# Kernel tuning notes

Measured on AMD Instinct MI355X. Metric: run time of the kernel, lower is better.

## Reference

```python
import jax, jax.numpy as jnp
import numpy as np

VOCAB = 1024   # must equal HID (embedding Linear consumes vocab-sized x)
HID = 1024
EMB = 256
NOS = 12
B, M = 512, 8
TEMP = 1.0


def setup_inputs() -> dict:
    key = jax.random.key(0)
    ks = jax.random.split(key, 12)
    N = B * M
    target = jax.random.normal(ks[0], (B, M, HID), jnp.float32)
    # precomputed standard Gumbel noise per step (training=True path)
    u = jax.random.uniform(ks[1], (NOS, N, VOCAB), jnp.float32, 1e-6, 1.0 - 1e-6)
    gumbels = -jnp.log(-jnp.log(u))
    sh = 1.0 / np.sqrt(HID)
    sv = 1.0 / np.sqrt(VOCAB)
    sos = 0.01 * jax.random.normal(ks[2], (EMB,), jnp.float32)
    W_ih = jax.random.uniform(ks[3], (HID, EMB), jnp.float32, -sh, sh)
    b_ih = jax.random.uniform(ks[4], (HID,), jnp.float32, -sh, sh)
    W_hh = jax.random.uniform(ks[5], (HID, HID), jnp.float32, -sh, sh)
    b_hh = jax.random.uniform(ks[6], (HID,), jnp.float32, -sh, sh)
    W_out = jax.random.uniform(ks[7], (VOCAB, HID), jnp.float32, -sh, sh)
    b_out = jax.random.uniform(ks[8], (VOCAB,), jnp.float32, -sh, sh)
    W_emb = jax.random.uniform(ks[9], (EMB, VOCAB), jnp.float32, -sv, sv)
    b_emb = jax.random.uniform(ks[10], (EMB,), jnp.float32, -sv, sv)
    return dict(target=target, gumbels=gumbels, sos=sos,
                W_ih=W_ih, b_ih=b_ih, W_hh=W_hh, b_hh=b_hh,
                W_out=W_out, b_out=b_out, W_emb=W_emb, b_emb=b_emb)


def reference(target, gumbels, sos, W_ih, b_ih, W_hh, b_hh, W_out, b_out, W_emb, b_emb):
    b_, m_, h_ = target.shape
    prev = target.reshape(b_ * m_, h_)            # [N, HID]
    e0 = jnp.broadcast_to(sos, (prev.shape[0], sos.shape[0]))  # [N, EMB]

    def step(carry, g):
        prev_h, e = carry
        h = jnp.tanh(e @ W_ih.T + b_ih + prev_h @ W_hh.T + b_hh)   # RNNCell
        logits = h @ W_out.T + b_out                               # [N, VOCAB]
        x = jax.nn.softmax((logits + g) / TEMP, axis=-1)           # gumbel-softmax
        e_next = x @ W_emb.T + b_emb                               # [N, EMB]
        return (h, e_next), x

    _, xs = jax.lax.scan(step, (prev, e0), gumbels)  # xs: [NOS, N, VOCAB]
    return jnp.transpose(xs, (1, 0, 2))              # [N, NOS, VOCAB]
```

## Files before the change

kernel.cpp:

```cpp
#include <hip/hip_runtime.h>

#define N_TOT 4096
#define HIDN  1024
#define EMBD  256
#define VOC   1024
#define NSTEP 12

typedef __bf16 bf16;
typedef _Float16 h16;
typedef __bf16 bf16x8 __attribute__((ext_vector_type(8)));
typedef __bf16 bf16x4 __attribute__((ext_vector_type(4)));
typedef _Float16 h16x8 __attribute__((ext_vector_type(8)));
typedef float  f32x4  __attribute__((ext_vector_type(4)));

static __device__ __forceinline__ f32x4 mfma16(bf16x8 a, bf16x8 b, f32x4 c) {
  return __builtin_amdgcn_mfma_f32_16x16x32_bf16(a, b, c, 0, 0, 0);
}

static __device__ __forceinline__ void gload16(const bf16* g, bf16* l) {
  __builtin_amdgcn_global_load_lds(
      (const __attribute__((address_space(1))) void*)g,
      (__attribute__((address_space(3))) void*)l, 16, 0, 0);
}


__global__ void cvt_kernel(const float* __restrict__ s, bf16* __restrict__ d, int n) {
  for (int i = blockIdx.x * blockDim.x + threadIdx.x; i < n; i += blockDim.x * gridDim.x)
    d[i] = (bf16)s[i];
}

__global__ void bias_sum_kernel(const float* __restrict__ a, const float* __restrict__ b,
                                float* __restrict__ c, int n) {
  int i = blockIdx.x * blockDim.x + threadIdx.x;
  if (i < n) c[i] = a[i] + b[i];
}

__global__ void fill_e_kernel(const float* __restrict__ sos, bf16* __restrict__ e) {
  for (int i = blockIdx.x * blockDim.x + threadIdx.x; i < N_TOT * EMBD;
       i += blockDim.x * gridDim.x)
    e[i] = (bf16)sos[i & (EMBD - 1)];
}


__global__ __launch_bounds__(256)
void rnn_cell_kernel(const bf16* __restrict__ e,
                     const bf16* __restrict__ hprev,
                     const bf16* __restrict__ Wih,
                     const bf16* __restrict__ Whh,
                     const float* __restrict__ bias,
                     bf16* __restrict__ hnew)
{
  __shared__ bf16 As[128 * 64];
  __shared__ bf16 Bs[64 * 64];
  const int tid = threadIdx.x;
  const int lane = tid & 63;
  const int w = tid >> 6;
  const int wr = w >> 1, wc = w & 1;
  const int id = (blockIdx.x & 7) * (gridDim.x >> 3) + (blockIdx.x >> 3);
  const int m0 = (id >> 4) * 128;
  const int n0 = (id & 15) * 64;
  const int lr = lane & 15, lk = lane >> 4;
  const int srow = lane >> 3;
  const int scol = (((lane & 7) ^ srow) << 3);

  f32x4 acc[4][2] = {};

  for (int phase = 0; phase < 2; ++phase) {
    const bf16* __restrict__ A = phase ? hprev : e;
    const bf16* __restrict__ B = phase ? Whh : Wih;
    const int K = phase ? HIDN : EMBD;
    for (int k0 = 0; k0 < K; k0 += 64) {
#pragma unroll
      for (int r = 0; r < 4; ++r)
        gload16(&A[(size_t)(m0 + r * 32 + w * 8 + srow) * K + k0 + scol],
                As + r * 2048 + w * 512);
#pragma unroll
      for (int r = 0; r < 2; ++r)
        gload16(&B[(size_t)(n0 + r * 32 + w * 8 + srow) * K + k0 + scol],
                Bs + r * 2048 + w * 512);
      __syncthreads();
#pragma unroll
      for (int kk = 0; kk < 2; ++kk) {
        bf16x8 af[4], bfr[2];
#pragma unroll
        for (int mi = 0; mi < 4; ++mi) {
          int row = wr * 64 + mi * 16 + lr;
          af[mi] = *(bf16x8*)&As[row * 64 + ((((kk << 2) | lk) ^ (row & 7)) << 3)];
        }
#pragma unroll
        for (int ni = 0; ni < 2; ++ni) {
          int row = wc * 32 + ni * 16 + lr;
          bfr[ni] = *(bf16x8*)&Bs[row * 64 + ((((kk << 2) | lk) ^ (row & 7)) << 3)];
        }
#pragma unroll
        for (int mi = 0; mi < 4; ++mi)
#pragma unroll
          for (int ni = 0; ni < 2; ++ni)
            acc[mi][ni] = mfma16(af[mi], bfr[ni], acc[mi][ni]);
      }
      __syncthreads();
    }
  }

#pragma unroll
  for (int mi = 0; mi < 4; ++mi) {
    int rowb = m0 + wr * 64 + mi * 16 + lk * 4;
#pragma unroll
    for (int ni = 0; ni < 2; ++ni) {
      int col = n0 + wc * 32 + ni * 16 + lr;
      float bs = bias[col];
#pragma unroll
      for (int j = 0; j < 4; ++j) {
        float v = tanhf(acc[mi][ni][j] + bs);
        hnew[(size_t)(rowb + j) * HIDN + col] = (bf16)v;
      }
    }
  }
}


__global__ __launch_bounds__(256)
void logits_kernel(const bf16* __restrict__ h,
                   const bf16* __restrict__ Wout,
                   const float* __restrict__ bout,
                   const float* __restrict__ gum,
                   h16* __restrict__ lbuf)
{
  __shared__ bf16 As[128 * 64];
  __shared__ bf16 Bs[64 * 64];
  const int tid = threadIdx.x;
  const int lane = tid & 63;
  const int w = tid >> 6;
  const int wr = w >> 1, wc = w & 1;
  const int id = (blockIdx.x & 7) * (gridDim.x >> 3) + (blockIdx.x >> 3);
  const int m0 = (id >> 4) * 128;
  const int n0 = (id & 15) * 64;
  const int lr = lane & 15, lk = lane >> 4;
  const int srow = lane >> 3;
  const int scol = (((lane & 7) ^ srow) << 3);

  f32x4 acc[4][2] = {};

  for (int k0 = 0; k0 < HIDN; k0 += 64) {
#pragma unroll
    for (int r = 0; r < 4; ++r)
      gload16(&h[(size_t)(m0 + r * 32 + w * 8 + srow) * HIDN + k0 + scol],
              As + r * 2048 + w * 512);
#pragma unroll
    for (int r = 0; r < 2; ++r)
      gload16(&Wout[(size_t)(n0 + r * 32 + w * 8 + srow) * HIDN + k0 + scol],
              Bs + r * 2048 + w * 512);
    __syncthreads();
#pragma unroll
    for (int kk = 0; kk < 2; ++kk) {
      bf16x8 af[4], bfr[2];
#pragma unroll
      for (int mi = 0; mi < 4; ++mi) {
        int row = wr * 64 + mi * 16 + lr;
        af[mi] = *(bf16x8*)&As[row * 64 + ((((kk << 2) | lk) ^ (row & 7)) << 3)];
      }
#pragma unroll
      for (int ni = 0; ni < 2; ++ni) {
        int row = wc * 32 + ni * 16 + lr;
        bfr[ni] = *(bf16x8*)&Bs[row * 64 + ((((kk << 2) | lk) ^ (row & 7)) << 3)];
      }
#pragma unroll
      for (int mi = 0; mi < 4; ++mi)
#pragma unroll
        for (int ni = 0; ni < 2; ++ni)
          acc[mi][ni] = mfma16(af[mi], bfr[ni], acc[mi][ni]);
    }
    __syncthreads();
  }

#pragma unroll
  for (int mi = 0; mi < 4; ++mi) {
    int rowb = m0 + wr * 64 + mi * 16 + lk * 4;
#pragma unroll
    for (int ni = 0; ni < 2; ++ni) {
      int col = n0 + wc * 32 + ni * 16 + lr;
      float bs = bout[col];
#pragma unroll
      for (int j = 0; j < 4; ++j) {
        int row = rowb + j;
        float v = acc[mi][ni][j] + bs + gum[(size_t)row * VOC + col];
        lbuf[(size_t)row * VOC + col] = (h16)v;
      }
    }
  }
}


__global__ __launch_bounds__(256)
void softmax_emb_kernel(const h16* __restrict__ lbuf,
                        const bf16* __restrict__ Wemb,
                        const float* __restrict__ bemb,
                        float* __restrict__ out,
                        bf16* __restrict__ enext,
                        int step)
{
  __shared__ bf16 xs[16 * 1032];
  const int tid = threadIdx.x;
  const int lane = tid & 63;
  const int w = tid >> 6;
  const int n0 = blockIdx.x * 16;

  for (int rr = 0; rr < 4; ++rr) {
    int r = w + rr * 4;
    const h16* rowp = lbuf + (size_t)(n0 + r) * VOC;
    float s[16];
    float m = -1e30f;
#pragma unroll
    for (int i = 0; i < 2; ++i) {
      h16x8 v = *(const h16x8*)&rowp[i * 512 + lane * 8];
#pragma unroll
      for (int j = 0; j < 8; ++j) {
        float f = (float)v[j];
        s[i * 8 + j] = f;
        m = fmaxf(m, f);
      }
    }
#pragma unroll
    for (int off = 32; off; off >>= 1) m = fmaxf(m, __shfl_xor(m, off));
    float sum = 0.f;
#pragma unroll
    for (int i = 0; i < 16; ++i) { s[i] = __expf(s[i] - m); sum += s[i]; }
#pragma unroll
    for (int off = 32; off; off >>= 1) sum += __shfl_xor(sum, off);
    float inv = 1.0f / sum;
    float* orow = out + ((size_t)(n0 + r) * NSTEP + step) * VOC;
#pragma unroll
    for (int i = 0; i < 2; ++i) {
      f32x4 v0, v1;
      bf16x8 bv;
#pragma unroll
      for (int j = 0; j < 4; ++j) {
        float x0 = s[i * 8 + j] * inv;
        float x1 = s[i * 8 + 4 + j] * inv;
        v0[j] = x0; v1[j] = x1;
        bv[j] = (bf16)x0; bv[4 + j] = (bf16)x1;
      }
      *(f32x4*)&orow[i * 512 + lane * 8] = v0;
      *(f32x4*)&orow[i * 512 + lane * 8 + 4] = v1;
      *(bf16x8*)&xs[r * 1032 + i * 512 + lane * 8] = bv;
    }
  }
  __syncthreads();

  const int lr = lane & 15, lk = lane >> 4;
  f32x4 acc[4] = {};
  for (int k0 = 0; k0 < VOC; k0 += 32) {
    bf16x8 a = *(bf16x8*)&xs[lr * 1032 + k0 + lk * 8];
#pragma unroll
    for (int ni = 0; ni < 4; ++ni) {
      int col = w * 64 + ni * 16 + lr;
      bf16x8 b = *(const bf16x8*)&Wemb[(size_t)col * VOC + k0 + lk * 8];
      acc[ni] = mfma16(a, b, acc[ni]);
    }
  }
#pragma unroll
  for (int ni = 0; ni < 4; ++ni) {
    int col = w * 64 + ni * 16 + lr;
    float bb = bemb[col];
#pragma unroll
    for (int j = 0; j < 4; ++j) {
      int n = n0 + lk * 4 + j;
      enext[(size_t)n * EMBD + col] = (bf16)(acc[ni][j] + bb);
    }
  }
}


extern "C" void kernel_launch(void* const* d_in, const int* in_sizes, int n_in,
                              void* d_out, int out_size, void* d_ws, size_t ws_size,
                              hipStream_t stream) {
  const float* target  = (const float*)d_in[0];
  const float* gumbels = (const float*)d_in[1];
  const float* sos     = (const float*)d_in[2];
  const float* W_ih    = (const float*)d_in[3];
  const float* b_ih    = (const float*)d_in[4];
  const float* W_hh    = (const float*)d_in[5];
  const float* b_hh    = (const float*)d_in[6];
  const float* W_out   = (const float*)d_in[7];
  const float* b_out   = (const float*)d_in[8];
  const float* W_emb   = (const float*)d_in[9];
  const float* b_emb   = (const float*)d_in[10];
  float* out = (float*)d_out;

  char* ws = (char*)d_ws;
  bf16* wih_b  = (bf16*)(ws);
  bf16* whh_b  = (bf16*)(ws + (1u << 20));
  bf16* wout_b = (bf16*)(ws + (3u << 20));
  bf16* wemb_b = (bf16*)(ws + (5u << 20));
  float* bias1 = (float*)(ws + (6u << 20));
  bf16* hbuf0  = (bf16*)(ws + (7u << 20));
  bf16* hbuf1  = (bf16*)(ws + (15u << 20));
  bf16* ebuf   = (bf16*)(ws + (23u << 20));
  h16*  lbuf   = (h16*) (ws + (25u << 20));

  auto cvt = [&](const float* s, bf16* d, int n) {
    int blocks = (n + 255) / 256; if (blocks > 2048) blocks = 2048;
    cvt_kernel<<<blocks, 256, 0, stream>>>(s, d, n);
  };
  cvt(W_ih,  wih_b,  HIDN * EMBD);
  cvt(W_hh,  whh_b,  HIDN * HIDN);
  cvt(W_out, wout_b, VOC * HIDN);
  cvt(W_emb, wemb_b, EMBD * VOC);
  cvt(target, hbuf0, N_TOT * HIDN);
  bias_sum_kernel<<<4, 256, 0, stream>>>(b_ih, b_hh, bias1, HIDN);
  fill_e_kernel<<<2048, 256, 0, stream>>>(sos, ebuf);

  bf16* hb[2] = {hbuf0, hbuf1};
  for (int t = 0; t < NSTEP; ++t) {
    bf16* hp = hb[t & 1];
    bf16* hn = hb[(t + 1) & 1];
    rnn_cell_kernel<<<(N_TOT / 128) * (HIDN / 64), 256, 0, stream>>>(
        ebuf, hp, wih_b, whh_b, bias1, hn);
    logits_kernel<<<(N_TOT / 128) * (VOC / 64), 256, 0, stream>>>(
        hn, wout_b, b_out, gumbels + (size_t)t * N_TOT * VOC, lbuf);
    softmax_emb_kernel<<<N_TOT / 16, 256, 0, stream>>>(
        lbuf, wemb_b, b_emb, out, ebuf, t);
  }
}
```

Before: 786.0 us.

## Double-buffer GEMM tiles, move gumbel add to softmax, fuse prep kernels

Both GEMM kernels now use double-buffered LDS tiles, so the next K-slice is loaded while the current one feeds the MFMAs, with one barrier per iteration instead of two. The Gumbel noise add moves from the logits epilogue into the softmax kernel, which reads fp32 noise with coalesced vector loads instead of scattered per-element reads. The softmax/embedding kernel goes to 512 threads so each wave handles fewer rows and output columns. The seven setup kernels are merged into one vectorised prep kernel. In exchange, the GEMMs use twice the LDS, which may lower occupancy.

New measurement: 753.1 us. 1.04x faster.

```diff
diff --git a/kernel.cpp b/kernel.cpp
--- a/kernel.cpp
+++ b/kernel.cpp
@@ -24,21 +24,39 @@
 }
 
 
-__global__ void cvt_kernel(const float* __restrict__ s, bf16* __restrict__ d, int n) {
-  for (int i = blockIdx.x * blockDim.x + threadIdx.x; i < n; i += blockDim.x * gridDim.x)
-    d[i] = (bf16)s[i];
-}
-
-__global__ void bias_sum_kernel(const float* __restrict__ a, const float* __restrict__ b,
-                                float* __restrict__ c, int n) {
-  int i = blockIdx.x * blockDim.x + threadIdx.x;
-  if (i < n) c[i] = a[i] + b[i];
-}
-
-__global__ void fill_e_kernel(const float* __restrict__ sos, bf16* __restrict__ e) {
-  for (int i = blockIdx.x * blockDim.x + threadIdx.x; i < N_TOT * EMBD;
-       i += blockDim.x * gridDim.x)
-    e[i] = (bf16)sos[i & (EMBD - 1)];
+__global__ void prep_kernel(const float* __restrict__ Wih, const float* __restrict__ Whh,
+                            const float* __restrict__ Wout, const float* __restrict__ Wemb,
+                            const float* __restrict__ target, const float* __restrict__ sos,
+                            const float* __restrict__ bih, const float* __restrict__ bhh,
+                            bf16* __restrict__ wih_b, bf16* __restrict__ whh_b,
+                            bf16* __restrict__ wout_b, bf16* __restrict__ wemb_b,
+                            bf16* __restrict__ hbuf, bf16* __restrict__ ebuf,
+                            float* __restrict__ bias1) {
+  for (int q = blockIdx.x * blockDim.x + threadIdx.x; q < 1966336;
+       q += blockDim.x * gridDim.x) {
+    if (q < 1703936) {
+      const float* s; bf16* d; int o;
+      if (q < 65536)        { s = Wih;    d = wih_b;  o = q; }
+      else if (q < 327680)  { s = Whh;    d = whh_b;  o = q - 65536; }
+      else if (q < 589824)  { s = Wout;   d = wout_b; o = q - 327680; }
+      else if (q < 655360)  { s = Wemb;   d = wemb_b; o = q - 589824; }
+      else                  { s = target; d = hbuf;   o = q - 655360; }
+      f32x4 v = *(const f32x4*)&s[(size_t)o * 4];
+      bf16x4 b; b[0] = (bf16)v.x; b[1] = (bf16)v.y; b[2] = (bf16)v.z; b[3] = (bf16)v.w;
+      *(bf16x4*)&d[(size_t)o * 4] = b;
+    } else if (q < 1966080) {
+      int o = q - 1703936;
+      f32x4 v = *(const f32x4*)&sos[(o & 63) * 4];
+      bf16x4 b; b[0] = (bf16)v.x; b[1] = (bf16)v.y; b[2] = (bf16)v.z; b[3] = (bf16)v.w;
+      *(bf16x4*)&ebuf[(size_t)o * 4] = b;
+    } else {
+      int o = q - 1966080;
+      f32x4 a = *(const f32x4*)&bih[o * 4];
+      f32x4 c = *(const f32x4*)&bhh[o * 4];
+      f32x4 r; r.x = a.x + c.x; r.y = a.y + c.y; r.z = a.z + c.z; r.w = a.w + c.w;
+      *(f32x4*)&bias1[o * 4] = r;
+    }
+  }
 }
 
 
@@ -50,8 +68,8 @@
                      const float* __restrict__ bias,
                      bf16* __restrict__ hnew)
 {
-  __shared__ bf16 As[128 * 64];
-  __shared__ bf16 Bs[64 * 64];
+  __shared__ bf16 As[2 * 128 * 64];
+  __shared__ bf16 Bs[2 * 64 * 64];
   const int tid = threadIdx.x;
   const int lane = tid & 63;
   const int w = tid >> 6;
@@ -63,43 +81,47 @@
   const int srow = lane >> 3;
   const int scol = (((lane & 7) ^ srow) << 3);
 
+  auto stage = [&](int t, int bsel) {
+    const bf16 *A, *B; int K, k0;
+    if (t < 4) { A = e;     B = Wih; K = EMBD; k0 = t << 6; }
+    else       { A = hprev; B = Whh; K = HIDN; k0 = (t - 4) << 6; }
+    bf16* Ad = As + bsel * 8192 + w * 512;
+    bf16* Bd = Bs + bsel * 4096 + w * 512;
+#pragma unroll
+    for (int r = 0; r < 4; ++r)
+      gload16(&A[(size_t)(m0 + r * 32 + w * 8 + srow) * K + k0 + scol], Ad + r * 2048);
+#pragma unroll
+    for (int r = 0; r < 2; ++r)
+      gload16(&B[(size_t)(n0 + r * 32 + w * 8 + srow) * K + k0 + scol], Bd + r * 2048);
+  };
+
   f32x4 acc[4][2] = {};
-
-  for (int phase = 0; phase < 2; ++phase) {
-    const bf16* __restrict__ A = phase ? hprev : e;
-    const bf16* __restrict__ B = phase ? Whh : Wih;
-    const int K = phase ? HIDN : EMBD;
-    for (int k0 = 0; k0 < K; k0 += 64) {
-#pragma unroll
-      for (int r = 0; r < 4; ++r)
-        gload16(&A[(size_t)(m0 + r * 32 + w * 8 + srow) * K + k0 + scol],
-                As + r * 2048 + w * 512);
-#pragma unroll
-      for (int r = 0; r < 2; ++r)
-        gload16(&B[(size_t)(n0 + r * 32 + w * 8 + srow) * K + k0 + scol],
-                Bs + r * 2048 + w * 512);
-      __syncthreads();
-#pragma unroll
-      for (int kk = 0; kk < 2; ++kk) {
-        bf16x8 af[4], bfr[2];
-#pragma unroll
-        for (int mi = 0; mi < 4; ++mi) {
-          int row = wr * 64 + mi * 16 + lr;
-          af[mi] = *(bf16x8*)&As[row * 64 + ((((kk << 2) | lk) ^ (row & 7)) << 3)];
-        }
-#pragma unroll
-        for (int ni = 0; ni < 2; ++ni) {
-          int row = wc * 32 + ni * 16 + lr;
-          bfr[ni] = *(bf16x8*)&Bs[row * 64 + ((((kk << 2) | lk) ^ (row & 7)) << 3)];
-        }
-#pragma unroll
-        for (int mi = 0; mi < 4; ++mi)
-#pragma unroll
-          for (int ni = 0; ni < 2; ++ni)
-            acc[mi][ni] = mfma16(af[mi], bfr[ni], acc[mi][ni]);
-      }
-      __syncthreads();
-    }
+  stage(0, 0);
+  __syncthreads();
+  for (int t = 0; t < 20; ++t) {
+    if (t < 19) stage(t + 1, (t + 1) & 1);
+    const bf16* Ab = As + (t & 1) * 8192;
+    const bf16* Bb = Bs + (t & 1) * 4096;
+#pragma unroll
+    for (int kk = 0; kk < 2; ++kk) {
+      bf16x8 af[4], bfr[2];
+#pragma unroll
+      for (int mi = 0; mi < 4; ++mi) {
+        int row = wr * 64 + mi * 16 + lr;
+        af[mi] = *(const bf16x8*)&Ab[row * 64 + ((((kk << 2) | lk) ^ (row & 7)) << 3)];
+      }
+#pragma unroll
+      for (int ni = 0; ni < 2; ++ni) {
+        int row = wc * 32 + ni * 16 + lr;
+        bfr[ni] = *(const bf16x8*)&Bb[row * 64 + ((((kk << 2) | lk) ^ (row & 7)) << 3)];
+      }
+#pragma unroll
+      for (int mi = 0; mi < 4; ++mi)
+#pragma unroll
+        for (int ni = 0; ni < 2; ++ni)
+          acc[mi][ni] = mfma16(af[mi], bfr[ni], acc[mi][ni]);
+    }
+    __syncthreads();
   }
 
 #pragma unroll
@@ -123,11 +145,10 @@
 void logits_kernel(const bf16* __restrict__ h,
                    const bf16* __restrict__ Wout,
                    const float* __restrict__ bout,
-                   const float* __restrict__ gum,
                    h16* __restrict__ lbuf)
 {
-  __shared__ bf16 As[128 * 64];
-  __shared__ bf16 Bs[64 * 64];
+  __shared__ bf16 As[2 * 128 * 64];
+  __shared__ bf16 Bs[2 * 64 * 64];
   const int tid = threadIdx.x;
   const int lane = tid & 63;
   const int w = tid >> 6;
@@ -139,30 +160,37 @@
   const int srow = lane >> 3;
   const int scol = (((lane & 7) ^ srow) << 3);
 
+  auto stage = [&](int t, int bsel) {
+    int k0 = t << 6;
+    bf16* Ad = As + bsel * 8192 + w * 512;
+    bf16* Bd = Bs + bsel * 4096 + w * 512;
+#pragma unroll
+    for (int r = 0; r < 4; ++r)
+      gload16(&h[(size_t)(m0 + r * 32 + w * 8 + srow) * HIDN + k0 + scol], Ad + r * 2048);
+#pragma unroll
+    for (int r = 0; r < 2; ++r)
+      gload16(&Wout[(size_t)(n0 + r * 32 + w * 8 + srow) * HIDN + k0 + scol], Bd + r * 2048);
+  };
+
   f32x4 acc[4][2] = {};
-
-  for (int k0 = 0; k0 < HIDN; k0 += 64) {
-#pragma unroll
-    for (int r = 0; r < 4; ++r)
-      gload16(&h[(size_t)(m0 + r * 32 + w * 8 + srow) * HIDN + k0 + scol],
-              As + r * 2048 + w * 512);
-#pragma unroll
-    for (int r = 0; r < 2; ++r)
-      gload16(&Wout[(size_t)(n0 + r * 32 + w * 8 + srow) * HIDN + k0 + scol],
-              Bs + r * 2048 + w * 512);
-    __syncthreads();
+  stage(0, 0);
+  __syncthreads();
+  for (int t = 0; t < 16; ++t) {
+    if (t < 15) stage(t + 1, (t + 1) & 1);
+    const bf16* Ab = As + (t & 1) * 8192;
+    const bf16* Bb = Bs + (t & 1) * 4096;
 #pragma unroll
     for (int kk = 0; kk < 2; ++kk) {
       bf16x8 af[4], bfr[2];
 #pragma unroll
       for (int mi = 0; mi < 4; ++mi) {
         int row = wr * 64 + mi * 16 + lr;
-        af[mi] = *(bf16x8*)&As[row * 64 + ((((kk << 2) | lk) ^ (row & 7)) << 3)];
+        af[mi] = *(const bf16x8*)&Ab[row * 64 + ((((kk << 2) | lk) ^ (row & 7)) << 3)];
       }
 #pragma unroll
       for (int ni = 0; ni < 2; ++ni) {
         int row = wc * 32 + ni * 16 + lr;
-        bfr[ni] = *(bf16x8*)&Bs[row * 64 + ((((kk << 2) | lk) ^ (row & 7)) << 3)];
+        bfr[ni] = *(const bf16x8*)&Bb[row * 64 + ((((kk << 2) | lk) ^ (row & 7)) << 3)];
       }
 #pragma unroll
       for (int mi = 0; mi < 4; ++mi)
@@ -183,16 +211,16 @@
 #pragma unroll
       for (int j = 0; j < 4; ++j) {
         int row = rowb + j;
-        float v = acc[mi][ni][j] + bs + gum[(size_t)row * VOC + col];
-        lbuf[(size_t)row * VOC + col] = (h16)v;
-      }
-    }
-  }
-}
-
-
-__global__ __launch_bounds__(256)
+        lbuf[(size_t)row * VOC + col] = (h16)(acc[mi][ni][j] + bs);
+      }
+    }
+  }
+}
+
+
+__global__ __launch_bounds__(512)
 void softmax_emb_kernel(const h16* __restrict__ lbuf,
+                        const float* __restrict__ gum,
                         const bf16* __restrict__ Wemb,
                         const float* __restrict__ bemb,
                         float* __restrict__ out,
@@ -205,19 +233,23 @@
   const int w = tid >> 6;
   const int n0 = blockIdx.x * 16;
 
-  for (int rr = 0; rr < 4; ++rr) {
-    int r = w + rr * 4;
-    const h16* rowp = lbuf + (size_t)(n0 + r) * VOC;
+  for (int rr = 0; rr < 2; ++rr) {
+    int r = w + rr * 8;
+    const h16* lrow = lbuf + (size_t)(n0 + r) * VOC;
+    const float* grow = gum + (size_t)(n0 + r) * VOC;
     float s[16];
     float m = -1e30f;
 #pragma unroll
     for (int i = 0; i < 2; ++i) {
-      h16x8 v = *(const h16x8*)&rowp[i * 512 + lane * 8];
-#pragma unroll
-      for (int j = 0; j < 8; ++j) {
-        float f = (float)v[j];
-        s[i * 8 + j] = f;
-        m = fmaxf(m, f);
+      h16x8 lv = *(const h16x8*)&lrow[i * 512 + lane * 8];
+      f32x4 g0 = *(const f32x4*)&grow[i * 512 + lane * 8];
+      f32x4 g1 = *(const f32x4*)&grow[i * 512 + lane * 8 + 4];
+#pragma unroll
+      for (int j = 0; j < 4; ++j) {
+        float f0 = (float)lv[j] + g0[j];
+        float f1 = (float)lv[4 + j] + g1[j];
+        s[i * 8 + j] = f0; s[i * 8 + 4 + j] = f1;
+        m = fmaxf(m, fmaxf(f0, f1));
       }
     }
 #pragma unroll
@@ -248,19 +280,19 @@
   __syncthreads();
 
   const int lr = lane & 15, lk = lane >> 4;
-  f32x4 acc[4] = {};
+  f32x4 acc[2] = {};
   for (int k0 = 0; k0 < VOC; k0 += 32) {
     bf16x8 a = *(bf16x8*)&xs[lr * 1032 + k0 + lk * 8];
 #pragma unroll
-    for (int ni = 0; ni < 4; ++ni) {
-      int col = w * 64 + ni * 16 + lr;
+    for (int ni = 0; ni < 2; ++ni) {
+      int col = w * 32 + ni * 16 + lr;
       bf16x8 b = *(const bf16x8*)&Wemb[(size_t)col * VOC + k0 + lk * 8];
       acc[ni] = mfma16(a, b, acc[ni]);
     }
   }
 #pragma unroll
-  for (int ni = 0; ni < 4; ++ni) {
-    int col = w * 64 + ni * 16 + lr;
+  for (int ni = 0; ni < 2; ++ni) {
+    int col = w * 32 + ni * 16 + lr;
     float bb = bemb[col];
 #pragma unroll
     for (int j = 0; j < 4; ++j) {
@@ -298,17 +330,9 @@
   bf16* ebuf   = (bf16*)(ws + (23u << 20));
   h16*  lbuf   = (h16*) (ws + (25u << 20));
 
-  auto cvt = [&](const float* s, bf16* d, int n) {
-    int blocks = (n + 255) / 256; if (blocks > 2048) blocks = 2048;
-    cvt_kernel<<<blocks, 256, 0, stream>>>(s, d, n);
-  };
-  cvt(W_ih,  wih_b,  HIDN * EMBD);
-  cvt(W_hh,  whh_b,  HIDN * HIDN);
-  cvt(W_out, wout_b, VOC * HIDN);
-  cvt(W_emb, wemb_b, EMBD * VOC);
-  cvt(target, hbuf0, N_TOT * HIDN);
-  bias_sum_kernel<<<4, 256, 0, stream>>>(b_ih, b_hh, bias1, HIDN);
-  fill_e_kernel<<<2048, 256, 0, stream>>>(sos, ebuf);
+  prep_kernel<<<2048, 256, 0, stream>>>(W_ih, W_hh, W_out, W_emb, target, sos,
+                                        b_ih, b_hh, wih_b, whh_b, wout_b, wemb_b,
+                                        hbuf0, ebuf, bias1);
 
   bf16* hb[2] = {hbuf0, hbuf1};
   for (int t = 0; t < NSTEP; ++t) {
@@ -317,8 +341,8 @@
     rnn_cell_kernel<<<(N_TOT / 128) * (HIDN / 64), 256, 0, stream>>>(
         ebuf, hp, wih_b, whh_b, bias1, hn);
     logits_kernel<<<(N_TOT / 128) * (VOC / 64), 256, 0, stream>>>(
-        hn, wout_b, b_out, gumbels + (size_t)t * N_TOT * VOC, lbuf);
-    softmax_emb_kernel<<<N_TOT / 16, 256, 0, stream>>>(
-        lbuf, wemb_b, b_emb, out, ebuf, t);
-  }
-}
+        hn, wout_b, b_out, lbuf);
+    softmax_emb_kernel<<<N_TOT / 16, 512, 0, stream>>>(
+        lbuf, gumbels + (size_t)t * N_TOT * VOC, wemb_b, b_emb, out, ebuf, t);
+  }
+}
```
